# Kernel optimization log

Measured on AMD Instinct MI355X. Metric: run time of the kernel, lower is better.

Reference implementation:

```python
import jax, jax.numpy as jnp
import numpy as np
import math

N_HEADS = 16
D_MODEL = 1024
D_K = D_MODEL // N_HEADS


def setup_inputs() -> dict:
    key = jax.random.key(0)
    ks = jax.random.split(key, 11)
    B, S = 4, 2048
    scale = 1.0 / math.sqrt(D_MODEL)
    return {
        "q": jax.random.normal(ks[0], (B, S, D_MODEL), jnp.float32),
        "k": jax.random.normal(ks[1], (B, S, D_MODEL), jnp.float32),
        "v": jax.random.normal(ks[2], (B, S, D_MODEL), jnp.float32),
        "Wq": jax.random.normal(ks[3], (D_MODEL, D_MODEL), jnp.float32) * scale,
        "bq": jax.random.normal(ks[4], (D_MODEL,), jnp.float32) * 0.01,
        "Wk": jax.random.normal(ks[5], (D_MODEL, D_MODEL), jnp.float32) * scale,
        "bk": jax.random.normal(ks[6], (D_MODEL,), jnp.float32) * 0.01,
        "Wv": jax.random.normal(ks[7], (D_MODEL, D_MODEL), jnp.float32) * scale,
        "bv": jax.random.normal(ks[8], (D_MODEL,), jnp.float32) * 0.01,
        "Wo": jax.random.normal(ks[9], (D_MODEL, D_MODEL), jnp.float32) * scale,
        "bo": jax.random.normal(ks[10], (D_MODEL,), jnp.float32) * 0.01,
    }


def reference(q, k, v, Wq, bq, Wk, bk, Wv, bv, Wo, bo):
    B, S, _ = q.shape
    # linear projections, then split heads: [B, H, S, d_k]
    def proj(x, W, b):
        y = x @ W.T + b
        return y.reshape(B, -1, N_HEADS, D_K).transpose(0, 2, 1, 3)
    qh = proj(q, Wq, bq)
    kh = proj(k, Wk, bk)
    vh = proj(v, Wv, bv)
    # scaled dot-product attention (mask=None, dropout p=0 -> identity)
    scores = jnp.einsum("bhqd,bhkd->bhqk", qh, kh) / math.sqrt(D_K)
    attn = jax.nn.softmax(scores, axis=-1)
    out = jnp.einsum("bhqk,bhkd->bhqd", attn, vh)  # [B, H, S, d_k]
    concat = out.transpose(0, 2, 1, 3).reshape(B, -1, D_MODEL)
    return concat @ Wo.T + bo
```

## Files before the change

kernel.cpp:

```cpp
#include <hip/hip_runtime.h>
#include <stdint.h>

#define DEVI __device__ __forceinline__

typedef __attribute__((ext_vector_type(8))) short bf16x8;
typedef __attribute__((ext_vector_type(4))) float f32x4;
typedef __attribute__((ext_vector_type(4))) int int4v;

DEVI unsigned short f2bf(float f) {
  union { float f; unsigned u; } v; v.f = f;
  return (unsigned short)((v.u + 0x7FFFu + ((v.u >> 16) & 1u)) >> 16);
}

__global__ __launch_bounds__(256) void cvt_kernel(const float* __restrict__ s,
                                                  unsigned short* __restrict__ d, int n) {
  int i = (blockIdx.x * 256 + threadIdx.x) * 4;
  if (i >= n) return;
  float4 v = *(const float4*)(s + i);
  union { unsigned short u[4]; uint2 w; } o;
  o.u[0] = f2bf(v.x); o.u[1] = f2bf(v.y); o.u[2] = f2bf(v.z); o.u[3] = f2bf(v.w);
  *(uint2*)(d + i) = o.w;
}

template<bool A_F32, bool OUT_HEADS>
__global__ __launch_bounds__(256) void gemm_bt(const void* __restrict__ Aptr,
                                               const unsigned short* __restrict__ Bmat,
                                               const float* __restrict__ bias,
                                               void* __restrict__ Cptr) {
  constexpr int K = 1024;
  constexpr int LDT = 72;
  __shared__ __align__(16) unsigned short Alds[128][LDT];
  __shared__ __align__(16) unsigned short Blds[128][LDT];
  const int tid = threadIdx.x;
  const int lane = tid & 63, w = tid >> 6;
  const int wm = w >> 1, wn = w & 1;
  const int l15 = lane & 15, lq = lane >> 4;
  const int rowBase = blockIdx.x * 128, colBase = blockIdx.y * 128;
  const int arow = tid >> 1, acol = (tid & 1) * 32;

  f32x4 acc[4][4] = {};

  float4 afp[8]; int4v abf[4]; int4v bbf[4];
  auto loadA = [&](int k0) {
    if (A_F32) {
      const float* p = (const float*)Aptr + (size_t)(rowBase + arow) * K + k0 + acol;
#pragma unroll
      for (int i = 0; i < 8; i++) afp[i] = *(const float4*)(p + i * 4);
    } else {
      const unsigned short* p = (const unsigned short*)Aptr + (size_t)(rowBase + arow) * K + k0 + acol;
#pragma unroll
      for (int i = 0; i < 4; i++) abf[i] = *(const int4v*)(p + i * 8);
    }
  };
  auto loadB = [&](int k0) {
    const unsigned short* p = Bmat + (size_t)(colBase + arow) * K + k0 + acol;
#pragma unroll
    for (int i = 0; i < 4; i++) bbf[i] = *(const int4v*)(p + i * 8);
  };

  loadA(0); loadB(0);

  for (int k0 = 0; k0 < K; k0 += 64) {
    __syncthreads();
    if (A_F32) {
      unsigned short t[32];
#pragma unroll
      for (int i = 0; i < 8; i++) {
        t[i*4+0] = f2bf(afp[i].x); t[i*4+1] = f2bf(afp[i].y);
        t[i*4+2] = f2bf(afp[i].z); t[i*4+3] = f2bf(afp[i].w);
      }
#pragma unroll
      for (int i = 0; i < 4; i++) *(int4v*)&Alds[arow][acol + i*8] = *(const int4v*)&t[i*8];
    } else {
#pragma unroll
      for (int i = 0; i < 4; i++) *(int4v*)&Alds[arow][acol + i*8] = abf[i];
    }
#pragma unroll
    for (int i = 0; i < 4; i++) *(int4v*)&Blds[arow][acol + i*8] = bbf[i];
    if (k0 + 64 < K) { loadA(k0 + 64); loadB(k0 + 64); }
    __syncthreads();
#pragma unroll
    for (int kc = 0; kc < 2; kc++) {
      bf16x8 af[4], bfr[4];
#pragma unroll
      for (int m = 0; m < 4; m++)
        af[m] = *(const bf16x8*)&Alds[wm*64 + m*16 + l15][kc*32 + lq*8];
#pragma unroll
      for (int n = 0; n < 4; n++)
        bfr[n] = *(const bf16x8*)&Blds[wn*64 + n*16 + l15][kc*32 + lq*8];
#pragma unroll
      for (int m = 0; m < 4; m++)
#pragma unroll
        for (int n = 0; n < 4; n++)
          acc[m][n] = __builtin_amdgcn_mfma_f32_16x16x32_bf16(af[m], bfr[n], acc[m][n], 0, 0, 0);
    }
  }
#pragma unroll
  for (int n = 0; n < 4; n++) {
    int col = colBase + wn*64 + n*16 + l15;
    float bv = bias[col];
#pragma unroll
    for (int m = 0; m < 4; m++) {
      int row0 = rowBase + wm*64 + m*16 + lq*4;
#pragma unroll
      for (int r = 0; r < 4; r++) {
        int row = row0 + r;
        float val = acc[m][n][r] + bv;
        if (OUT_HEADS) {
          unsigned short* C = (unsigned short*)Cptr;
          int hh = col >> 6, dd = col & 63;
          int bb = row >> 11, ss = row & 2047;
          C[(((size_t)(bb*16 + hh)*2048 + ss) << 6) + dd] = f2bf(val);
        } else {
          ((float*)Cptr)[(size_t)row * 1024 + col] = val;
        }
      }
    }
  }
}

__global__ __launch_bounds__(256) void attn_kernel(const unsigned short* __restrict__ Qh,
                                                   const unsigned short* __restrict__ Kh,
                                                   const unsigned short* __restrict__ Vh,
                                                   unsigned short* __restrict__ Obuf) {
  constexpr int LDT = 72;
  __shared__ __align__(16) unsigned short Klds[64][LDT];
  __shared__ __align__(16) unsigned short Vt[64][LDT];
  __shared__ __align__(16) unsigned short Plds[4][32][LDT];
  const int tid = threadIdx.x;
  const int lane = tid & 63, w = tid >> 6;
  const int l15 = lane & 15, lq = lane >> 4;
  const int bh = blockIdx.y;
  const int qbase = blockIdx.x * 128 + w * 32;
  const unsigned short* Qp = Qh + (size_t)bh * 2048 * 64;
  const unsigned short* Kp = Kh + (size_t)bh * 2048 * 64;
  const unsigned short* Vp = Vh + (size_t)bh * 2048 * 64;

  bf16x8 qf[2][2];
#pragma unroll
  for (int mi = 0; mi < 2; mi++)
#pragma unroll
    for (int kc = 0; kc < 2; kc++)
      qf[mi][kc] = *(const bf16x8*)(Qp + (size_t)(qbase + mi*16 + l15) * 64 + kc*32 + lq*8);

  f32x4 oacc[2][4] = {};
  float mrun[2][4], lrun[2][4];
#pragma unroll
  for (int mi = 0; mi < 2; mi++)
#pragma unroll
    for (int r = 0; r < 4; r++) { mrun[mi][r] = -1e30f; lrun[mi][r] = 0.f; }

  const int krow = tid >> 2, kcol = (tid & 3) * 16;
  int4v kreg[2], vreg[2];
  auto loadKV = [&](int kt) {
    const unsigned short* ks = Kp + (size_t)(kt + krow) * 64 + kcol;
    kreg[0] = *(const int4v*)ks; kreg[1] = *(const int4v*)(ks + 8);
    const unsigned short* vs = Vp + (size_t)(kt + krow) * 64 + kcol;
    vreg[0] = *(const int4v*)vs; vreg[1] = *(const int4v*)(vs + 8);
  };
  loadKV(0);

  for (int kt = 0; kt < 2048; kt += 64) {
    __syncthreads();
    *(int4v*)&Klds[krow][kcol]     = kreg[0];
    *(int4v*)&Klds[krow][kcol + 8] = kreg[1];
    {
      union { int4v v[2]; unsigned short u[16]; } tv;
      tv.v[0] = vreg[0]; tv.v[1] = vreg[1];
#pragma unroll
      for (int e = 0; e < 16; e++) Vt[kcol + e][krow] = tv.u[e];
    }
    if (kt + 64 < 2048) loadKV(kt + 64);
    __syncthreads();

    f32x4 sf[2][4] = {};
#pragma unroll
    for (int kc = 0; kc < 2; kc++) {
      bf16x8 bfr[4];
#pragma unroll
      for (int n = 0; n < 4; n++)
        bfr[n] = *(const bf16x8*)&Klds[n*16 + l15][kc*32 + lq*8];
#pragma unroll
      for (int mi = 0; mi < 2; mi++)
#pragma unroll
        for (int n = 0; n < 4; n++)
          sf[mi][n] = __builtin_amdgcn_mfma_f32_16x16x32_bf16(qf[mi][kc], bfr[n], sf[mi][n], 0, 0, 0);
    }
#pragma unroll
    for (int mi = 0; mi < 2; mi++) {
#pragma unroll
      for (int r = 0; r < 4; r++) {
        float s0 = sf[mi][0][r] * 0.125f, s1 = sf[mi][1][r] * 0.125f;
        float s2 = sf[mi][2][r] * 0.125f, s3 = sf[mi][3][r] * 0.125f;
        float tm = fmaxf(fmaxf(s0, s1), fmaxf(s2, s3));
        tm = fmaxf(tm, __shfl_xor(tm, 1)); tm = fmaxf(tm, __shfl_xor(tm, 2));
        tm = fmaxf(tm, __shfl_xor(tm, 4)); tm = fmaxf(tm, __shfl_xor(tm, 8));
        float mold = mrun[mi][r];
        float mnew = fmaxf(mold, tm);
        float alpha = __expf(mold - mnew);
        mrun[mi][r] = mnew;
        float p0 = __expf(s0 - mnew), p1 = __expf(s1 - mnew);
        float p2 = __expf(s2 - mnew), p3 = __expf(s3 - mnew);
        float ts = p0 + p1 + p2 + p3;
        ts += __shfl_xor(ts, 1); ts += __shfl_xor(ts, 2);
        ts += __shfl_xor(ts, 4); ts += __shfl_xor(ts, 8);
        lrun[mi][r] = lrun[mi][r] * alpha + ts;
#pragma unroll
        for (int n = 0; n < 4; n++) oacc[mi][n][r] *= alpha;
        int prow = mi*16 + lq*4 + r;
        Plds[w][prow][l15]      = f2bf(p0);
        Plds[w][prow][l15 + 16] = f2bf(p1);
        Plds[w][prow][l15 + 32] = f2bf(p2);
        Plds[w][prow][l15 + 48] = f2bf(p3);
      }
    }
#pragma unroll
    for (int kc = 0; kc < 2; kc++) {
      bf16x8 pa[2], vb[4];
#pragma unroll
      for (int mi = 0; mi < 2; mi++)
        pa[mi] = *(const bf16x8*)&Plds[w][mi*16 + l15][kc*32 + lq*8];
#pragma unroll
      for (int n = 0; n < 4; n++)
        vb[n] = *(const bf16x8*)&Vt[n*16 + l15][kc*32 + lq*8];
#pragma unroll
      for (int mi = 0; mi < 2; mi++)
#pragma unroll
        for (int n = 0; n < 4; n++)
          oacc[mi][n] = __builtin_amdgcn_mfma_f32_16x16x32_bf16(pa[mi], vb[n], oacc[mi][n], 0, 0, 0);
    }
  }
  const int b = bh >> 4, h = bh & 15;
#pragma unroll
  for (int mi = 0; mi < 2; mi++) {
#pragma unroll
    for (int r = 0; r < 4; r++) {
      float inv = 1.0f / lrun[mi][r];
      int q = qbase + mi*16 + lq*4 + r;
#pragma unroll
      for (int n = 0; n < 4; n++)
        Obuf[((size_t)b*2048 + q)*1024 + h*64 + n*16 + l15] = f2bf(oacc[mi][n][r] * inv);
    }
  }
}

extern "C" void kernel_launch(void* const* d_in, const int* in_sizes, int n_in,
                              void* d_out, int out_size, void* d_ws, size_t ws_size,
                              hipStream_t stream) {
  const float* q  = (const float*)d_in[0];
  const float* k  = (const float*)d_in[1];
  const float* v  = (const float*)d_in[2];
  const float* Wq = (const float*)d_in[3];
  const float* bq = (const float*)d_in[4];
  const float* Wk = (const float*)d_in[5];
  const float* bk = (const float*)d_in[6];
  const float* Wv = (const float*)d_in[7];
  const float* bv = (const float*)d_in[8];
  const float* Wo = (const float*)d_in[9];
  const float* bo = (const float*)d_in[10];

  unsigned short* Wqb = (unsigned short*)d_ws;
  unsigned short* Wkb = Wqb + 1024*1024;
  unsigned short* Wvb = Wkb + 1024*1024;
  unsigned short* Wob = Wvb + 1024*1024;
  unsigned short* Qh  = Wob + 1024*1024;
  unsigned short* Kh  = Qh + (size_t)8192*1024;
  unsigned short* Vh  = Kh + (size_t)8192*1024;
  unsigned short* Ob  = Vh + (size_t)8192*1024;

  cvt_kernel<<<1024, 256, 0, stream>>>(Wq, Wqb, 1024*1024);
  cvt_kernel<<<1024, 256, 0, stream>>>(Wk, Wkb, 1024*1024);
  cvt_kernel<<<1024, 256, 0, stream>>>(Wv, Wvb, 1024*1024);
  cvt_kernel<<<1024, 256, 0, stream>>>(Wo, Wob, 1024*1024);

  dim3 g(64, 8), blk(256);
  gemm_bt<true, true><<<g, blk, 0, stream>>>(q, Wqb, bq, Qh);
  gemm_bt<true, true><<<g, blk, 0, stream>>>(k, Wkb, bk, Kh);
  gemm_bt<true, true><<<g, blk, 0, stream>>>(v, Wvb, bv, Vh);

  attn_kernel<<<dim3(16, 64), blk, 0, stream>>>(Qh, Kh, Vh, Ob);

  gemm_bt<false, false><<<g, blk, 0, stream>>>(Ob, Wob, bo, (float*)d_out);
}
```

Baseline: 562.5 us.

## Rewrite attention kernel as register-resident flash attention with pre-transposed V

```diff
diff --git a/kernel.cpp b/kernel.cpp
--- a/kernel.cpp
+++ b/kernel.cpp
@@ -22,11 +22,11 @@
   *(uint2*)(d + i) = o.w;
 }
 
-template<bool A_F32, bool OUT_HEADS>
+template<bool A_F32, int OUT_MODE>
 __global__ __launch_bounds__(256) void gemm_bt(const void* __restrict__ Aptr,
                                                const unsigned short* __restrict__ Bmat,
                                                const float* __restrict__ bias,
-                                               void* __restrict__ Cptr) {
+                                               void* __restrict__ Cptr, float oscale) {
   constexpr int K = 1024;
   constexpr int LDT = 72;
   __shared__ __align__(16) unsigned short Alds[128][LDT];
@@ -105,141 +105,170 @@
 #pragma unroll
       for (int r = 0; r < 4; r++) {
         int row = row0 + r;
-        float val = acc[m][n][r] + bv;
-        if (OUT_HEADS) {
+        float val = (acc[m][n][r] + bv) * oscale;
+        if (OUT_MODE == 0) {
+          ((float*)Cptr)[(size_t)row * 1024 + col] = val;
+        } else {
           unsigned short* C = (unsigned short*)Cptr;
           int hh = col >> 6, dd = col & 63;
           int bb = row >> 11, ss = row & 2047;
-          C[(((size_t)(bb*16 + hh)*2048 + ss) << 6) + dd] = f2bf(val);
-        } else {
-          ((float*)Cptr)[(size_t)row * 1024 + col] = val;
+          int bh = bb * 16 + hh;
+          if (OUT_MODE == 1) C[(((size_t)bh * 2048 + ss) << 6) + dd] = f2bf(val);
+          else               C[((size_t)bh << 17) + ((size_t)dd << 11) + ss] = f2bf(val);
         }
       }
     }
   }
 }
 
-__global__ __launch_bounds__(256) void attn_kernel(const unsigned short* __restrict__ Qh,
-                                                   const unsigned short* __restrict__ Kh,
-                                                   const unsigned short* __restrict__ Vh,
-                                                   unsigned short* __restrict__ Obuf) {
-  constexpr int LDT = 72;
-  __shared__ __align__(16) unsigned short Klds[64][LDT];
-  __shared__ __align__(16) unsigned short Vt[64][LDT];
-  __shared__ __align__(16) unsigned short Plds[4][32][LDT];
-  const int tid = threadIdx.x;
-  const int lane = tid & 63, w = tid >> 6;
+__global__ __launch_bounds__(256, 2) void attn_kernel(const unsigned short* __restrict__ Qh,
+                                                      const unsigned short* __restrict__ Kh,
+                                                      const unsigned short* __restrict__ VT,
+                                                      unsigned short* __restrict__ Ob) {
+  const int tid = threadIdx.x, lane = tid & 63, w = tid >> 6;
   const int l15 = lane & 15, lq = lane >> 4;
-  const int bh = blockIdx.y;
-  const int qbase = blockIdx.x * 128 + w * 32;
-  const unsigned short* Qp = Qh + (size_t)bh * 2048 * 64;
-  const unsigned short* Kp = Kh + (size_t)bh * 2048 * 64;
-  const unsigned short* Vp = Vh + (size_t)bh * 2048 * 64;
-
-  bf16x8 qf[2][2];
+  const int bid = blockIdx.x;
+  const int xcd = bid & 7, slot = bid >> 3;
+  const int bh = xcd * 8 + (slot >> 4), qt = slot & 15;
+  const int qbase = qt * 128 + w * 32;
+  const unsigned short* Qp = Qh + ((size_t)bh << 17);
+  const unsigned short* Kp = Kh + ((size_t)bh << 17);
+  const unsigned short* Vp = VT + ((size_t)bh << 17);
+
+  bf16x8 qb[2][2];
 #pragma unroll
   for (int mi = 0; mi < 2; mi++)
 #pragma unroll
     for (int kc = 0; kc < 2; kc++)
-      qf[mi][kc] = *(const bf16x8*)(Qp + (size_t)(qbase + mi*16 + l15) * 64 + kc*32 + lq*8);
+      qb[mi][kc] = *(const bf16x8*)(Qp + (size_t)(qbase + mi*16 + l15) * 64 + kc*32 + lq*8);
 
   f32x4 oacc[2][4] = {};
-  float mrun[2][4], lrun[2][4];
-#pragma unroll
-  for (int mi = 0; mi < 2; mi++)
-#pragma unroll
-    for (int r = 0; r < 4; r++) { mrun[mi][r] = -1e30f; lrun[mi][r] = 0.f; }
-
-  const int krow = tid >> 2, kcol = (tid & 3) * 16;
-  int4v kreg[2], vreg[2];
-  auto loadKV = [&](int kt) {
-    const unsigned short* ks = Kp + (size_t)(kt + krow) * 64 + kcol;
-    kreg[0] = *(const int4v*)ks; kreg[1] = *(const int4v*)(ks + 8);
-    const unsigned short* vs = Vp + (size_t)(kt + krow) * 64 + kcol;
-    vreg[0] = *(const int4v*)vs; vreg[1] = *(const int4v*)(vs + 8);
+  float mrun[2] = {-1e30f, -1e30f};
+  float lrun[2] = {0.f, 0.f};
+
+  bf16x8 kaA[4][2], kaB[4][2];
+  auto loadK = [&](bf16x8 (&ka)[4][2], int kt) {
+#pragma unroll
+    for (int kb = 0; kb < 4; kb++)
+#pragma unroll
+      for (int kc = 0; kc < 2; kc++)
+        ka[kb][kc] = *(const bf16x8*)(Kp + (size_t)(kt + kb*16 + l15) * 64 + kc*32 + lq*8);
   };
-  loadKV(0);
-
-  for (int kt = 0; kt < 2048; kt += 64) {
-    __syncthreads();
-    *(int4v*)&Klds[krow][kcol]     = kreg[0];
-    *(int4v*)&Klds[krow][kcol + 8] = kreg[1];
-    {
-      union { int4v v[2]; unsigned short u[16]; } tv;
-      tv.v[0] = vreg[0]; tv.v[1] = vreg[1];
-#pragma unroll
-      for (int e = 0; e < 16; e++) Vt[kcol + e][krow] = tv.u[e];
-    }
-    if (kt + 64 < 2048) loadKV(kt + 64);
-    __syncthreads();
+  loadK(kaA, 0);
+
+  auto tile = [&](bf16x8 (&ka)[4][2], bf16x8 (&kan)[4][2], int kt, int ktn) {
+    bf16x8 va[4][2];
+#pragma unroll
+    for (int db = 0; db < 4; db++)
+#pragma unroll
+      for (int win = 0; win < 2; win++)
+        va[db][win] = *(const bf16x8*)(Vp + (size_t)(db*16 + l15) * 2048 + kt + win*32 + lq*8);
 
     f32x4 sf[2][4] = {};
 #pragma unroll
-    for (int kc = 0; kc < 2; kc++) {
-      bf16x8 bfr[4];
-#pragma unroll
-      for (int n = 0; n < 4; n++)
-        bfr[n] = *(const bf16x8*)&Klds[n*16 + l15][kc*32 + lq*8];
+    for (int kc = 0; kc < 2; kc++)
 #pragma unroll
       for (int mi = 0; mi < 2; mi++)
 #pragma unroll
-        for (int n = 0; n < 4; n++)
-          sf[mi][n] = __builtin_amdgcn_mfma_f32_16x16x32_bf16(qf[mi][kc], bfr[n], sf[mi][n], 0, 0, 0);
-    }
+        for (int kb = 0; kb < 4; kb++)
+          sf[mi][kb] = __builtin_amdgcn_mfma_f32_16x16x32_bf16(ka[kb][kc], qb[mi][kc], sf[mi][kb], 0, 0, 0);
+
+    if (ktn < 2048) loadK(kan, ktn);
+
+    float pm[2];
 #pragma unroll
     for (int mi = 0; mi < 2; mi++) {
-#pragma unroll
-      for (int r = 0; r < 4; r++) {
-        float s0 = sf[mi][0][r] * 0.125f, s1 = sf[mi][1][r] * 0.125f;
-        float s2 = sf[mi][2][r] * 0.125f, s3 = sf[mi][3][r] * 0.125f;
-        float tm = fmaxf(fmaxf(s0, s1), fmaxf(s2, s3));
-        tm = fmaxf(tm, __shfl_xor(tm, 1)); tm = fmaxf(tm, __shfl_xor(tm, 2));
-        tm = fmaxf(tm, __shfl_xor(tm, 4)); tm = fmaxf(tm, __shfl_xor(tm, 8));
-        float mold = mrun[mi][r];
-        float mnew = fmaxf(mold, tm);
-        float alpha = __expf(mold - mnew);
-        mrun[mi][r] = mnew;
-        float p0 = __expf(s0 - mnew), p1 = __expf(s1 - mnew);
-        float p2 = __expf(s2 - mnew), p3 = __expf(s3 - mnew);
-        float ts = p0 + p1 + p2 + p3;
-        ts += __shfl_xor(ts, 1); ts += __shfl_xor(ts, 2);
-        ts += __shfl_xor(ts, 4); ts += __shfl_xor(ts, 8);
-        lrun[mi][r] = lrun[mi][r] * alpha + ts;
-#pragma unroll
-        for (int n = 0; n < 4; n++) oacc[mi][n][r] *= alpha;
-        int prow = mi*16 + lq*4 + r;
-        Plds[w][prow][l15]      = f2bf(p0);
-        Plds[w][prow][l15 + 16] = f2bf(p1);
-        Plds[w][prow][l15 + 32] = f2bf(p2);
-        Plds[w][prow][l15 + 48] = f2bf(p3);
-      }
-    }
-#pragma unroll
-    for (int kc = 0; kc < 2; kc++) {
-      bf16x8 pa[2], vb[4];
-#pragma unroll
-      for (int mi = 0; mi < 2; mi++)
-        pa[mi] = *(const bf16x8*)&Plds[w][mi*16 + l15][kc*32 + lq*8];
-#pragma unroll
-      for (int n = 0; n < 4; n++)
-        vb[n] = *(const bf16x8*)&Vt[n*16 + l15][kc*32 + lq*8];
-#pragma unroll
-      for (int mi = 0; mi < 2; mi++)
-#pragma unroll
-        for (int n = 0; n < 4; n++)
-          oacc[mi][n] = __builtin_amdgcn_mfma_f32_16x16x32_bf16(pa[mi], vb[n], oacc[mi][n], 0, 0, 0);
-    }
+      float t0 = fmaxf(fmaxf(sf[mi][0][0], sf[mi][0][1]), fmaxf(sf[mi][0][2], sf[mi][0][3]));
+      float t1 = fmaxf(fmaxf(sf[mi][1][0], sf[mi][1][1]), fmaxf(sf[mi][1][2], sf[mi][1][3]));
+      float t2 = fmaxf(fmaxf(sf[mi][2][0], sf[mi][2][1]), fmaxf(sf[mi][2][2], sf[mi][2][3]));
+      float t3 = fmaxf(fmaxf(sf[mi][3][0], sf[mi][3][1]), fmaxf(sf[mi][3][2], sf[mi][3][3]));
+      float t = fmaxf(fmaxf(t0, t1), fmaxf(t2, t3));
+      t = fmaxf(t, __shfl_xor(t, 16));
+      t = fmaxf(t, __shfl_xor(t, 32));
+      pm[mi] = t;
+    }
+    if (__any((pm[0] > mrun[0] + 11.5f) || (pm[1] > mrun[1] + 11.5f))) {
+#pragma unroll
+      for (int mi = 0; mi < 2; mi++) {
+        float mnew = fmaxf(mrun[mi], pm[mi]);
+        float alpha = __builtin_amdgcn_exp2f(mrun[mi] - mnew);
+        mrun[mi] = mnew; lrun[mi] *= alpha;
+#pragma unroll
+        for (int db = 0; db < 4; db++)
+#pragma unroll
+          for (int r = 0; r < 4; r++) oacc[mi][db][r] *= alpha;
+      }
+    }
+#pragma unroll
+    for (int mi = 0; mi < 2; mi++) {
+      float s = 0.f;
+#pragma unroll
+      for (int kb = 0; kb < 4; kb++)
+#pragma unroll
+        for (int r = 0; r < 4; r++) {
+          float e = __builtin_amdgcn_exp2f(sf[mi][kb][r] - mrun[mi]);
+          sf[mi][kb][r] = e; s += e;
+        }
+      s += __shfl_xor(s, 16);
+      s += __shfl_xor(s, 32);
+      lrun[mi] += s;
+    }
+
+    const int half = lq >> 1;
+    const unsigned selp = (unsigned)((lq ^ half) & 1);
+#pragma unroll
+    for (int mi = 0; mi < 2; mi++) {
+      bf16x8 pb[2];
+#pragma unroll
+      for (int win = 0; win < 2; win++) {
+        unsigned u00, u01, u10, u11;
+        asm("v_cvt_pk_bf16_f32 %0, %1, %2" : "=v"(u00) : "v"(sf[mi][2*win][0]),   "v"(sf[mi][2*win][1]));
+        asm("v_cvt_pk_bf16_f32 %0, %1, %2" : "=v"(u01) : "v"(sf[mi][2*win][2]),   "v"(sf[mi][2*win][3]));
+        asm("v_cvt_pk_bf16_f32 %0, %1, %2" : "=v"(u10) : "v"(sf[mi][2*win+1][0]), "v"(sf[mi][2*win+1][1]));
+        asm("v_cvt_pk_bf16_f32 %0, %1, %2" : "=v"(u11) : "v"(sf[mi][2*win+1][2]), "v"(sf[mi][2*win+1][3]));
+        unsigned lw0 = half ? u10 : u00, lw1 = half ? u11 : u01;
+        unsigned sa0 = half ? u00 : u10, sa1 = half ? u01 : u11;
+        unsigned y0 = (unsigned)__shfl_xor((int)sa0, 32);
+        unsigned y1 = (unsigned)__shfl_xor((int)sa1, 32);
+        unsigned z0 = selp ? lw0 : y0, z1 = selp ? lw1 : y1;
+        unsigned r0 = (unsigned)__shfl_xor((int)z0, 16);
+        unsigned r1 = (unsigned)__shfl_xor((int)z1, 16);
+        unsigned wl0 = (lq == 0) ? lw0 : ((lq == 2) ? y0 : r0);
+        unsigned wl1 = (lq == 0) ? lw1 : ((lq == 2) ? y1 : r1);
+        unsigned wh0 = (lq == 3) ? lw0 : ((lq == 1) ? y0 : r0);
+        unsigned wh1 = (lq == 3) ? lw1 : ((lq == 1) ? y1 : r1);
+        union { unsigned u[4]; bf16x8 v; } pf;
+        pf.u[0] = wl0; pf.u[1] = wl1; pf.u[2] = wh0; pf.u[3] = wh1;
+        pb[win] = pf.v;
+      }
+#pragma unroll
+      for (int db = 0; db < 4; db++) {
+        oacc[mi][db] = __builtin_amdgcn_mfma_f32_16x16x32_bf16(va[db][0], pb[0], oacc[mi][db], 0, 0, 0);
+        oacc[mi][db] = __builtin_amdgcn_mfma_f32_16x16x32_bf16(va[db][1], pb[1], oacc[mi][db], 0, 0, 0);
+      }
+    }
+  };
+
+  for (int kt = 0; kt < 2048; kt += 128) {
+    tile(kaA, kaB, kt, kt + 64);
+    tile(kaB, kaA, kt + 64, kt + 128);
   }
+
   const int b = bh >> 4, h = bh & 15;
 #pragma unroll
   for (int mi = 0; mi < 2; mi++) {
-#pragma unroll
-    for (int r = 0; r < 4; r++) {
-      float inv = 1.0f / lrun[mi][r];
-      int q = qbase + mi*16 + lq*4 + r;
-#pragma unroll
-      for (int n = 0; n < 4; n++)
-        Obuf[((size_t)b*2048 + q)*1024 + h*64 + n*16 + l15] = f2bf(oacc[mi][n][r] * inv);
+    const float inv = 1.0f / lrun[mi];
+    const int q = qbase + mi*16 + l15;
+    const size_t base = ((size_t)b * 2048 + q) * 1024 + h * 64;
+#pragma unroll
+    for (int db = 0; db < 4; db++) {
+      float e0 = oacc[mi][db][0] * inv, e1 = oacc[mi][db][1] * inv;
+      float e2 = oacc[mi][db][2] * inv, e3 = oacc[mi][db][3] * inv;
+      unsigned w0, w1;
+      asm("v_cvt_pk_bf16_f32 %0, %1, %2" : "=v"(w0) : "v"(e0), "v"(e1));
+      asm("v_cvt_pk_bf16_f32 %0, %1, %2" : "=v"(w1) : "v"(e2), "v"(e3));
+      uint2 st; st.x = w0; st.y = w1;
+      *(uint2*)(Ob + base + db*16 + lq*4) = st;
     }
   }
 }
@@ -260,25 +289,27 @@
   const float* bo = (const float*)d_in[10];
 
   unsigned short* Wqb = (unsigned short*)d_ws;
-  unsigned short* Wkb = Wqb + 1024*1024;
-  unsigned short* Wvb = Wkb + 1024*1024;
-  unsigned short* Wob = Wvb + 1024*1024;
-  unsigned short* Qh  = Wob + 1024*1024;
-  unsigned short* Kh  = Qh + (size_t)8192*1024;
-  unsigned short* Vh  = Kh + (size_t)8192*1024;
-  unsigned short* Ob  = Vh + (size_t)8192*1024;
-
-  cvt_kernel<<<1024, 256, 0, stream>>>(Wq, Wqb, 1024*1024);
-  cvt_kernel<<<1024, 256, 0, stream>>>(Wk, Wkb, 1024*1024);
-  cvt_kernel<<<1024, 256, 0, stream>>>(Wv, Wvb, 1024*1024);
-  cvt_kernel<<<1024, 256, 0, stream>>>(Wo, Wob, 1024*1024);
+  unsigned short* Wkb = Wqb + 1024 * 1024;
+  unsigned short* Wvb = Wkb + 1024 * 1024;
+  unsigned short* Wob = Wvb + 1024 * 1024;
+  unsigned short* Ob  = Wob + 1024 * 1024;
+  unsigned short* Qh  = Ob + (size_t)8192 * 1024;
+  unsigned short* Kh  = Qh + (size_t)8192 * 1024;
+  unsigned short* VT  = Kh + (size_t)8192 * 1024;
+
+  const float QSCALE = 0.125f * 1.44269504f;
+
+  cvt_kernel<<<1024, 256, 0, stream>>>(Wq, Wqb, 1024 * 1024);
+  cvt_kernel<<<1024, 256, 0, stream>>>(Wk, Wkb, 1024 * 1024);
+  cvt_kernel<<<1024, 256, 0, stream>>>(Wv, Wvb, 1024 * 1024);
+  cvt_kernel<<<1024, 256, 0, stream>>>(Wo, Wob, 1024 * 1024);
 
   dim3 g(64, 8), blk(256);
-  gemm_bt<true, true><<<g, blk, 0, stream>>>(q, Wqb, bq, Qh);
-  gemm_bt<true, true><<<g, blk, 0, stream>>>(k, Wkb, bk, Kh);
-  gemm_bt<true, true><<<g, blk, 0, stream>>>(v, Wvb, bv, Vh);
-
-  attn_kernel<<<dim3(16, 64), blk, 0, stream>>>(Qh, Kh, Vh, Ob);
-
-  gemm_bt<false, false><<<g, blk, 0, stream>>>(Ob, Wob, bo, (float*)d_out);
-}
+  gemm_bt<true, 1><<<g, blk, 0, stream>>>(q, Wqb, bq, Qh, QSCALE);
+  gemm_bt<true, 1><<<g, blk, 0, stream>>>(k, Wkb, bk, Kh, 1.0f);
+  gemm_bt<true, 2><<<g, blk, 0, stream>>>(v, Wvb, bv, VT, 1.0f);
+
+  attn_kernel<<<dim3(1024), blk, 0, stream>>>(Qh, Kh, VT, Ob);
+
+  gemm_bt<false, 0><<<g, blk, 0, stream>>>(Ob, Wob, bo, (float*)d_out, 1.0f);
+}
```

After: 545.8 us. 3.0% less time.
